# Kernel optimization log

Hardware: AMD Instinct MI355X
Metric: run time of the kernel (lower is better)

## Reference

```python
import jax, jax.numpy as jnp
import numpy as np

B, N, E = 16, 4096, 65536
IN, H = 256, 512
G1, G2 = 32, 32
M1, M2 = 1024, 32768
GOD = 8
BN_EPS = 1e-5


def setup_inputs() -> dict:
    key = jax.random.key(0)
    ks = jax.random.split(key, 16)
    rn = lambda i, sh, s=0.05: jax.random.normal(ks[i], sh, dtype=jnp.float32) * s
    return {
        "x": jax.random.normal(ks[0], (B, IN), dtype=jnp.float32),
        "smoothed_vert_pos": jax.random.normal(ks[1], (B, N * 3), dtype=jnp.float32),
        "hidden": jnp.zeros((B, H), jnp.float32),
        "edge_index": jax.random.randint(ks[2], (2, E), 0, N),
        "W0": rn(3, (G1, 3), 0.3), "a0_src": rn(4, (G1,), 0.3), "a0_dst": rn(5, (G1,), 0.3), "b0": jnp.zeros((G1,), jnp.float32),
        "W1": rn(6, (G2, G1), 0.2), "a1_src": rn(7, (G2,), 0.2), "a1_dst": rn(8, (G2,), 0.2), "b1": jnp.zeros((G2,), jnp.float32),
        "w_ih": rn(9, (3 * H, IN)), "w_hh": rn(10, (3 * H, H)),
        "b_ih": jnp.zeros((3 * H,), jnp.float32), "b_hh": jnp.zeros((3 * H,), jnp.float32),
        "lin1_w": rn(11, (M1, H)), "lin1_b": jnp.zeros((M1,), jnp.float32),
        "prelu1": jnp.full((M1,), 0.25, jnp.float32), "bn1_g": jnp.ones((M1,), jnp.float32), "bn1_b": jnp.zeros((M1,), jnp.float32),
        "lin2_w": rn(12, (M2, M1), 0.02), "lin2_b": jnp.zeros((M2,), jnp.float32),
        "prelu2": jnp.full((M2,), 0.25, jnp.float32), "bn2_g": jnp.ones((M2,), jnp.float32), "bn2_b": jnp.zeros((M2,), jnp.float32),
        "w_out": rn(13, (3, G2 + GOD), 0.2), "b_out": jnp.zeros((3,), jnp.float32),
    }


def _gat(v, src, dst, W, a_s, a_d, b):
    # PyG GATConv, heads=1, eval mode (no dropout), self-loops already in src/dst
    h = v @ W.T                                           # [N, F]
    e = jax.nn.leaky_relu((h * a_s).sum(-1)[src] + (h * a_d).sum(-1)[dst], 0.2)  # [E+N]
    m = jax.ops.segment_max(e, dst, num_segments=N)       # segment-softmax over incoming edges
    w = jnp.exp(e - m[dst])
    s = jax.ops.segment_sum(w, dst, num_segments=N)
    coef = w / s[dst]
    return jax.ops.segment_sum(coef[:, None] * h[src], dst, num_segments=N) + b


def _mlp_layer(t, w, bb, p, g, be):
    t = t @ w.T + bb                                      # Linear
    t = jnp.where(t >= 0, t, p * t)                       # PReLU (per-channel)
    # eval BatchNorm1d with running_mean=0, running_var=1
    return (t / jnp.sqrt(1.0 + BN_EPS)) * g + be


def reference(x, smoothed_vert_pos, hidden, edge_index,
              W0, a0_src, a0_dst, b0, W1, a1_src, a1_dst, b1,
              w_ih, w_hh, b_ih, b_hh,
              lin1_w, lin1_b, prelu1, bn1_g, bn1_b,
              lin2_w, lin2_b, prelu2, bn2_g, bn2_b,
              w_out, b_out):
    sv = smoothed_vert_pos.reshape(B, N, 3)
    loop = jnp.arange(N, dtype=edge_index.dtype)
    src = jnp.concatenate([edge_index[0], loop])          # GATConv add_self_loops=True
    dst = jnp.concatenate([edge_index[1], loop])
    gat0 = jax.vmap(lambda v: _gat(v, src, dst, W0, a0_src, a0_dst, b0))(sv)   # [B,N,G1]
    gat1 = jax.vmap(lambda v: _gat(v, src, dst, W1, a1_src, a1_dst, b1))(gat0)  # [B,N,G2]

    # GRUCell
    gi = x @ w_ih.T + b_ih
    gh = hidden @ w_hh.T + b_hh
    ir, iz, inn = jnp.split(gi, 3, axis=-1)
    hr, hz, hn = jnp.split(gh, 3, axis=-1)
    r = jax.nn.sigmoid(ir + hr)
    z = jax.nn.sigmoid(iz + hz)
    n = jnp.tanh(inn + r * hn)
    next_hidden = (1.0 - z) * n + z * hidden              # [B,H]

    o = _mlp_layer(next_hidden, lin1_w, lin1_b, prelu1, bn1_g, bn1_b)
    o = _mlp_layer(o, lin2_w, lin2_b, prelu2, bn2_g, bn2_b)
    gru_out = o.reshape(B, N, GOD)

    y = (jnp.concatenate([gru_out, gat1], axis=2) @ w_out.T + b_out).reshape(B, -1)
    return y, next_hidden
```

## Files before the change

### kernel.cpp

```cpp
#include <hip/hip_runtime.h>

#define BB 16
#define NN 4096
#define EE 65536
#define HH 512
#define M1N 1024
#define M2N 32768
#define CAP 96



__global__ void k_pre(int* __restrict__ cnt,
                      const float* __restrict__ x, const float* __restrict__ hid,
                      const float* __restrict__ w_ih, const float* __restrict__ w_hh,
                      const float* __restrict__ b_ih, const float* __restrict__ b_hh,
                      float* __restrict__ nh, float* __restrict__ out_nh,
                      const float* __restrict__ svp, const float* __restrict__ W0,
                      const float* __restrict__ a0s, const float* __restrict__ a0d,
                      float* __restrict__ h0t, float* __restrict__ as0t,
                      float* __restrict__ ad0t) {
  const int bid = blockIdx.x;
  if (bid < 16) {
    cnt[bid * 256 + threadIdx.x] = 0;
    return;
  }
  if (bid < 2064) {
    int wid = (bid - 16) * 4 + (threadIdx.x >> 6);
    int lane = threadIdx.x & 63;
    int b = wid >> 9, j = wid & 511;
    const float* xb = x + b * 256;
    const float* hb = hid + b * HH;
    float ir = 0.f, iz = 0.f, in_ = 0.f, hr = 0.f, hz = 0.f, hn = 0.f;
    for (int k = lane; k < 256; k += 64) {
      float xv = xb[k];
      ir  += xv * w_ih[(size_t)j * 256 + k];
      iz  += xv * w_ih[(size_t)(j + 512) * 256 + k];
      in_ += xv * w_ih[(size_t)(j + 1024) * 256 + k];
    }
    for (int k = lane; k < 512; k += 64) {
      float hv = hb[k];
      hr += hv * w_hh[(size_t)j * 512 + k];
      hz += hv * w_hh[(size_t)(j + 512) * 512 + k];
      hn += hv * w_hh[(size_t)(j + 1024) * 512 + k];
    }
#pragma unroll
    for (int m = 1; m < 64; m <<= 1) {
      ir += __shfl_xor(ir, m, 64); iz += __shfl_xor(iz, m, 64); in_ += __shfl_xor(in_, m, 64);
      hr += __shfl_xor(hr, m, 64); hz += __shfl_xor(hz, m, 64); hn  += __shfl_xor(hn, m, 64);
    }
    if (lane == 0) {
      ir += b_ih[j]; iz += b_ih[j + 512]; in_ += b_ih[j + 1024];
      hr += b_hh[j]; hz += b_hh[j + 512]; hn += b_hh[j + 1024];
      float r = 1.f / (1.f + __expf(-(ir + hr)));
      float z = 1.f / (1.f + __expf(-(iz + hz)));
      float n = tanhf(in_ + r * hn);
      float v = (1.f - z) * n + z * hb[j];
      nh[wid] = v;
      out_nh[wid] = v;
    }
    return;
  }
  int gid = (bid - 2064) * 256 + threadIdx.x;
  int grp = gid >> 5, f = gid & 31;
  int b = grp >> 12, n = grp & 4095;
  const float* v = svp + (size_t)grp * 3;
  float hv = v[0] * W0[f * 3] + v[1] * W0[f * 3 + 1] + v[2] * W0[f * 3 + 2];
  h0t[(size_t)n * 512 + b * 32 + f] = hv;
  float ps = hv * a0s[f], pd = hv * a0d[f];
#pragma unroll
  for (int m = 1; m < 32; m <<= 1) {
    ps += __shfl_xor(ps, m, 64);
    pd += __shfl_xor(pd, m, 64);
  }
  if (f == 0) { as0t[n * 16 + b] = ps; ad0t[n * 16 + b] = pd; }
}


__global__ void k_fill2(const int* __restrict__ src, const int* __restrict__ dst,
                        int* __restrict__ cnt, int* __restrict__ csr) {
  int k = blockIdx.x * 256 + threadIdx.x;
  if (k < EE) {
    int d = dst[k];
    int slot = atomicAdd(&cnt[d], 1);
    if ((unsigned)slot < CAP) csr[d * CAP + slot] = src[k];
  }
}


__global__ void k_mid(const int* __restrict__ cnt, const int* __restrict__ csr,
                      const float* __restrict__ h0t, const float* __restrict__ as0t,
                      const float* __restrict__ ad0t, const float* __restrict__ b0,
                      const float* __restrict__ W1, const float* __restrict__ a1s,
                      const float* __restrict__ a1d,
                      float* __restrict__ h1t, float* __restrict__ as1t,
                      float* __restrict__ ad1t,
                      const float* __restrict__ nh, const float* __restrict__ l1w,
                      const float* __restrict__ l1b, const float* __restrict__ p1,
                      const float* __restrict__ g1v, const float* __restrict__ be1,
                      float* __restrict__ o1) {
  const int bid = blockIdx.x;
  const int wave = threadIdx.x >> 6;
  const int lane = threadIdx.x & 63;
  if (bid < 2048) {
    __shared__ float lds[4][8][36];
    const int n  = bid * 2 + (wave >> 1);
    const int bh = wave & 1;
    const int bl = lane >> 3;
    const int fq = lane & 7;
    const int b  = bh * 8 + bl;
    const int f0 = fq * 4;
    const int deg = min(cnt[n], CAP);
    const int base = n * CAP;
    const float adn = ad0t[n * 16 + b];
    const int total = deg + 1;
    float4 acc = {0.f, 0.f, 0.f, 0.f};
    float asum = 0.f;
    for (int i = 0; i < total; i += 4) {
      int sv0, sv1, sv2, sv3;
      {
        int r0 = csr[base + i];
        int r1 = csr[base + i + 1];
        int r2 = csr[base + i + 2];
        int r3 = csr[base + i + 3];
        sv0 = (i     < deg) ? r0 : n;
        sv1 = (i + 1 < deg) ? r1 : n;
        sv2 = (i + 2 < deg) ? r2 : n;
        sv3 = (i + 3 < deg) ? r3 : n;
      }
      float e0 = as0t[sv0 * 16 + b];
      float e1 = as0t[sv1 * 16 + b];
      float e2 = as0t[sv2 * 16 + b];
      float e3 = as0t[sv3 * 16 + b];
      float4 hv0 = *(const float4*)(h0t + (size_t)sv0 * 512 + b * 32 + f0);
      float4 hv1 = *(const float4*)(h0t + (size_t)sv1 * 512 + b * 32 + f0);
      float4 hv2 = *(const float4*)(h0t + (size_t)sv2 * 512 + b * 32 + f0);
      float4 hv3 = *(const float4*)(h0t + (size_t)sv3 * 512 + b * 32 + f0);
      float e, w;
      e = e0 + adn; e = e >= 0.f ? e : 0.2f * e;
      w = (i     < total) ? __expf(e) : 0.f;
      asum += w; acc.x += w*hv0.x; acc.y += w*hv0.y; acc.z += w*hv0.z; acc.w += w*hv0.w;
      e = e1 + adn; e = e >= 0.f ? e : 0.2f * e;
      w = (i + 1 < total) ? __expf(e) : 0.f;
      asum += w; acc.x += w*hv1.x; acc.y += w*hv1.y; acc.z += w*hv1.z; acc.w += w*hv1.w;
      e = e2 + adn; e = e >= 0.f ? e : 0.2f * e;
      w = (i + 2 < total) ? __expf(e) : 0.f;
      asum += w; acc.x += w*hv2.x; acc.y += w*hv2.y; acc.z += w*hv2.z; acc.w += w*hv2.w;
      e = e3 + adn; e = e >= 0.f ? e : 0.2f * e;
      w = (i + 3 < total) ? __expf(e) : 0.f;
      asum += w; acc.x += w*hv3.x; acc.y += w*hv3.y; acc.z += w*hv3.z; acc.w += w*hv3.w;
    }
    float inv = 1.f / asum;
    float4 b0v = *(const float4*)(b0 + f0);
    float4 g0;
    g0.x = acc.x * inv + b0v.x; g0.y = acc.y * inv + b0v.y;
    g0.z = acc.z * inv + b0v.z; g0.w = acc.w * inv + b0v.w;
    *(float4*)&lds[wave][bl][f0] = g0;
    __syncthreads();
    float h1a = 0.f, h1b = 0.f, h1c = 0.f, h1d = 0.f;
    const float* gr = lds[wave][bl];
    const float* w1r = W1 + f0 * 32;
#pragma unroll
    for (int k = 0; k < 32; ++k) {
      float gk = gr[k];
      h1a += gk * w1r[k];
      h1b += gk * w1r[32 + k];
      h1c += gk * w1r[64 + k];
      h1d += gk * w1r[96 + k];
    }
    float4 h1v = {h1a, h1b, h1c, h1d};
    *(float4*)(h1t + (size_t)n * 512 + b * 32 + f0) = h1v;
    float ps = h1a * a1s[f0] + h1b * a1s[f0+1] + h1c * a1s[f0+2] + h1d * a1s[f0+3];
    float pd = h1a * a1d[f0] + h1b * a1d[f0+1] + h1c * a1d[f0+2] + h1d * a1d[f0+3];
#pragma unroll
    for (int m = 1; m < 8; m <<= 1) {
      ps += __shfl_xor(ps, m, 64);
      pd += __shfl_xor(pd, m, 64);
    }
    if (fq == 0) { as1t[n * 16 + b] = ps; ad1t[n * 16 + b] = pd; }
    return;
  }
  int wid = (bid - 2048) * 4 + wave;
  int b = wid >> 10, j = wid & 1023;
  const float* hb = nh + b * HH;
  const float* wr = l1w + (size_t)j * HH;
  float acc = 0.f;
  for (int k = lane; k < HH; k += 64) acc += hb[k] * wr[k];
#pragma unroll
  for (int m = 1; m < 64; m <<= 1) acc += __shfl_xor(acc, m, 64);
  if (lane == 0) {
    float t = acc + l1b[j];
    t = t >= 0.f ? t : p1[j] * t;
    o1[wid] = t * 0.99999500003749973f * g1v[j] + be1[j];
  }
}


__global__ __launch_bounds__(256, 4) void k_lin2(
    const float* __restrict__ o1, const float* __restrict__ w,
    const float* __restrict__ bias, const float* __restrict__ pr,
    const float* __restrict__ g, const float* __restrict__ be,
    float* __restrict__ o2) {
  const int wave = threadIdx.x >> 6;
  const int lane = threadIdx.x & 63;
  const int bh = lane >> 5;
  const int kl = lane & 31;
  const int j0 = (blockIdx.x * 4 + wave) * 4;
  const float* ob = o1 + (size_t)bh * 8 * 1024;
  const float* w0 = w + (size_t)j0 * 1024;
  float acc[4][8];
#pragma unroll
  for (int r = 0; r < 4; r++)
#pragma unroll
    for (int b = 0; b < 8; b++) acc[r][b] = 0.f;
#pragma unroll 1
  for (int it = 0; it < 8; ++it) {
    const int kq = it * 128 + kl * 4;
    float4 wv0 = *(const float4*)(w0 + kq);
    float4 wv1 = *(const float4*)(w0 + 1024 + kq);
    float4 wv2 = *(const float4*)(w0 + 2048 + kq);
    float4 wv3 = *(const float4*)(w0 + 3072 + kq);
#pragma unroll
    for (int b = 0; b < 8; b++) {
      float4 v = *(const float4*)(ob + b * 1024 + kq);
      acc[0][b] += wv0.x*v.x + wv0.y*v.y + wv0.z*v.z + wv0.w*v.w;
      acc[1][b] += wv1.x*v.x + wv1.y*v.y + wv1.z*v.z + wv1.w*v.w;
      acc[2][b] += wv2.x*v.x + wv2.y*v.y + wv2.z*v.z + wv2.w*v.w;
      acc[3][b] += wv3.x*v.x + wv3.y*v.y + wv3.z*v.z + wv3.w*v.w;
    }
  }
#pragma unroll
  for (int r = 0; r < 4; r++)
#pragma unroll
    for (int b = 0; b < 8; b++)
#pragma unroll
      for (int m = 1; m < 32; m <<= 1)
        acc[r][b] += __shfl_xor(acc[r][b], m, 64);
  if (kl == 0) {
    const float INV = 0.99999500003749973f;
#pragma unroll
    for (int r = 0; r < 4; r++) {
      const int j = j0 + r;
      const float bj = bias[j], pj = pr[j], gj = g[j], bej = be[j];
#pragma unroll
      for (int b = 0; b < 8; b++) {
        float t = acc[r][b] + bj;
        t = t >= 0.f ? t : pj * t;
        o2[(size_t)(bh * 8 + b) * M2N + j] = t * INV * gj + bej;
      }
    }
  }
}


__global__ void k_fin(const int* __restrict__ cnt, const int* __restrict__ csr,
                      const float* __restrict__ h1t, const float* __restrict__ as1t,
                      const float* __restrict__ ad1t, const float* __restrict__ b1,
                      const float* __restrict__ o2, const float* __restrict__ wout,
                      const float* __restrict__ bout, float* __restrict__ y) {
  const int wave = threadIdx.x >> 6;
  const int lane = threadIdx.x & 63;
  const int n  = blockIdx.x * 2 + (wave >> 1);
  const int bh = wave & 1;
  const int bl = lane >> 3;
  const int fq = lane & 7;
  const int b  = bh * 8 + bl;
  const int f0 = fq * 4;
  const int deg = min(cnt[n], CAP);
  const int base = n * CAP;
  const float adn = ad1t[n * 16 + b];
  const int total = deg + 1;
  float4 acc = {0.f, 0.f, 0.f, 0.f};
  float asum = 0.f;
  for (int i = 0; i < total; i += 4) {
    int sv0, sv1, sv2, sv3;
    {
      int r0 = csr[base + i];
      int r1 = csr[base + i + 1];
      int r2 = csr[base + i + 2];
      int r3 = csr[base + i + 3];
      sv0 = (i     < deg) ? r0 : n;
      sv1 = (i + 1 < deg) ? r1 : n;
      sv2 = (i + 2 < deg) ? r2 : n;
      sv3 = (i + 3 < deg) ? r3 : n;
    }
    float e0 = as1t[sv0 * 16 + b];
    float e1 = as1t[sv1 * 16 + b];
    float e2 = as1t[sv2 * 16 + b];
    float e3 = as1t[sv3 * 16 + b];
    float4 hv0 = *(const float4*)(h1t + (size_t)sv0 * 512 + b * 32 + f0);
    float4 hv1 = *(const float4*)(h1t + (size_t)sv1 * 512 + b * 32 + f0);
    float4 hv2 = *(const float4*)(h1t + (size_t)sv2 * 512 + b * 32 + f0);
    float4 hv3 = *(const float4*)(h1t + (size_t)sv3 * 512 + b * 32 + f0);
    float e, w;
    e = e0 + adn; e = e >= 0.f ? e : 0.2f * e;
    w = (i     < total) ? __expf(e) : 0.f;
    asum += w; acc.x += w*hv0.x; acc.y += w*hv0.y; acc.z += w*hv0.z; acc.w += w*hv0.w;
    e = e1 + adn; e = e >= 0.f ? e : 0.2f * e;
    w = (i + 1 < total) ? __expf(e) : 0.f;
    asum += w; acc.x += w*hv1.x; acc.y += w*hv1.y; acc.z += w*hv1.z; acc.w += w*hv1.w;
    e = e2 + adn; e = e >= 0.f ? e : 0.2f * e;
    w = (i + 2 < total) ? __expf(e) : 0.f;
    asum += w; acc.x += w*hv2.x; acc.y += w*hv2.y; acc.z += w*hv2.z; acc.w += w*hv2.w;
    e = e3 + adn; e = e >= 0.f ? e : 0.2f * e;
    w = (i + 3 < total) ? __expf(e) : 0.f;
    asum += w; acc.x += w*hv3.x; acc.y += w*hv3.y; acc.z += w*hv3.z; acc.w += w*hv3.w;
  }
  float inv = 1.f / asum;
  float4 b1v = *(const float4*)(b1 + f0);
  float gx = acc.x * inv + b1v.x, gy = acc.y * inv + b1v.y;
  float gz = acc.z * inv + b1v.z, gw = acc.w * inv + b1v.w;
  float pc0 = gx*wout[ 8+f0] + gy*wout[ 9+f0] + gz*wout[10+f0] + gw*wout[11+f0];
  float pc1 = gx*wout[48+f0] + gy*wout[49+f0] + gz*wout[50+f0] + gw*wout[51+f0];
  float pc2 = gx*wout[88+f0] + gy*wout[89+f0] + gz*wout[90+f0] + gw*wout[91+f0];
#pragma unroll
  for (int m = 1; m < 8; m <<= 1) {
    pc0 += __shfl_xor(pc0, m, 64);
    pc1 += __shfl_xor(pc1, m, 64);
    pc2 += __shfl_xor(pc2, m, 64);
  }
  if (fq == 0) {
    const float* gr = o2 + (size_t)b * M2N + n * 8;
    float4 ga = *(const float4*)gr;
    float4 gb = *(const float4*)(gr + 4);
    float c0 = pc0 + bout[0], c1 = pc1 + bout[1], c2 = pc2 + bout[2];
    c0 += ga.x*wout[0]  + ga.y*wout[1]  + ga.z*wout[2]  + ga.w*wout[3]
        + gb.x*wout[4]  + gb.y*wout[5]  + gb.z*wout[6]  + gb.w*wout[7];
    c1 += ga.x*wout[40] + ga.y*wout[41] + ga.z*wout[42] + ga.w*wout[43]
        + gb.x*wout[44] + gb.y*wout[45] + gb.z*wout[46] + gb.w*wout[47];
    c2 += ga.x*wout[80] + ga.y*wout[81] + ga.z*wout[82] + ga.w*wout[83]
        + gb.x*wout[84] + gb.y*wout[85] + gb.z*wout[86] + gb.w*wout[87];
    float* yp = y + (size_t)b * (NN * 3) + n * 3;
    yp[0] = c0; yp[1] = c1; yp[2] = c2;
  }
}


extern "C" void kernel_launch(void* const* d_in, const int* in_sizes, int n_in,
                              void* d_out, int out_size, void* d_ws, size_t ws_size,
                              hipStream_t stream) {
  const float* x    = (const float*)d_in[0];
  const float* svp  = (const float*)d_in[1];
  const float* hid  = (const float*)d_in[2];
  const int*   ei   = (const int*)d_in[3];
  const float* W0   = (const float*)d_in[4];
  const float* a0s  = (const float*)d_in[5];
  const float* a0d  = (const float*)d_in[6];
  const float* b0   = (const float*)d_in[7];
  const float* W1   = (const float*)d_in[8];
  const float* a1s  = (const float*)d_in[9];
  const float* a1d  = (const float*)d_in[10];
  const float* b1   = (const float*)d_in[11];
  const float* w_ih = (const float*)d_in[12];
  const float* w_hh = (const float*)d_in[13];
  const float* b_ih = (const float*)d_in[14];
  const float* b_hh = (const float*)d_in[15];
  const float* l1w  = (const float*)d_in[16];
  const float* l1b  = (const float*)d_in[17];
  const float* p1   = (const float*)d_in[18];
  const float* g1v  = (const float*)d_in[19];
  const float* be1  = (const float*)d_in[20];
  const float* l2w  = (const float*)d_in[21];
  const float* l2b  = (const float*)d_in[22];
  const float* p2   = (const float*)d_in[23];
  const float* g2v  = (const float*)d_in[24];
  const float* be2  = (const float*)d_in[25];
  const float* wout = (const float*)d_in[26];
  const float* bout = (const float*)d_in[27];
  float* out = (float*)d_out;

  char* ws = (char*)d_ws;
  size_t off = 0;
  auto alloc = [&](size_t bytes) -> char* {
    char* p = ws + off;
    off += (bytes + 255) & ~(size_t)255;
    return p;
  };
  int*   cnt   = (int*)alloc((size_t)NN * 4);
  int*   csr   = (int*)alloc(((size_t)NN * CAP + 16) * 4);
  float* h0t   = (float*)alloc((size_t)NN * 16 * 32 * 4);
  float* as0t  = (float*)alloc((size_t)NN * 16 * 4);
  float* ad0t  = (float*)alloc((size_t)NN * 16 * 4);
  float* h1t   = (float*)alloc((size_t)NN * 16 * 32 * 4);
  float* as1t  = (float*)alloc((size_t)NN * 16 * 4);
  float* ad1t  = (float*)alloc((size_t)NN * 16 * 4);
  float* nh    = (float*)alloc((size_t)BB * HH * 4);
  float* o1    = (float*)alloc((size_t)BB * M1N * 4);
  float* o2    = (float*)alloc((size_t)BB * M2N * 4);

  const int* srcv = ei;
  const int* dstv = ei + EE;

  k_pre<<<16 + 2048 + 8192, 256, 0, stream>>>(
      cnt, x, hid, w_ih, w_hh, b_ih, b_hh, nh, out + (size_t)BB * NN * 3,
      svp, W0, a0s, a0d, h0t, as0t, ad0t);
  k_fill2<<<EE / 256, 256, 0, stream>>>(srcv, dstv, cnt, csr);
  k_mid<<<2048 + 4096, 256, 0, stream>>>(
      cnt, csr, h0t, as0t, ad0t, b0, W1, a1s, a1d, h1t, as1t, ad1t,
      nh, l1w, l1b, p1, g1v, be1, o1);
  k_lin2<<<M2N / 16, 256, 0, stream>>>(o1, l2w, l2b, p2, g2v, be2, o2);
  k_fin<<<2048, 256, 0, stream>>>(cnt, csr, h1t, as1t, ad1t, b1, o2, wout, bout, out);
}
```

Baseline: 127.2 us.

## Regroup independent stages into fewer kernels to cut launch count

Reorganizes the kernel schedule. The lin1 GEMV now shares a kernel with CSR fill. The lin2 GEMV shares a kernel with GAT layer 0 aggregation. This takes the pipeline from five launches to four and lets independent branches overlap within each launch. The cost is that k_mid2 now applies launch_bounds(256,4) and shared memory to the GAT blocks too, which may constrain registers or occupancy for that branch.

```diff
diff --git a/kernel.cpp b/kernel.cpp
--- a/kernel.cpp
+++ b/kernel.cpp
@@ -76,9 +76,32 @@
 }
 
 
-__global__ void k_fill2(const int* __restrict__ src, const int* __restrict__ dst,
-                        int* __restrict__ cnt, int* __restrict__ csr) {
-  int k = blockIdx.x * 256 + threadIdx.x;
+__global__ void k_mid1(const float* __restrict__ nh, const float* __restrict__ l1w,
+                       const float* __restrict__ l1b, const float* __restrict__ p1,
+                       const float* __restrict__ g1v, const float* __restrict__ be1,
+                       float* __restrict__ o1,
+                       const int* __restrict__ src, const int* __restrict__ dst,
+                       int* __restrict__ cnt, int* __restrict__ csr) {
+  const int bid = blockIdx.x;
+  if (bid < 4096) {
+    const int wave = threadIdx.x >> 6;
+    const int lane = threadIdx.x & 63;
+    int wid = bid * 4 + wave;
+    int b = wid >> 10, j = wid & 1023;
+    const float* hb = nh + b * HH;
+    const float* wr = l1w + (size_t)j * HH;
+    float acc = 0.f;
+    for (int k = lane; k < HH; k += 64) acc += hb[k] * wr[k];
+#pragma unroll
+    for (int m = 1; m < 64; m <<= 1) acc += __shfl_xor(acc, m, 64);
+    if (lane == 0) {
+      float t = acc + l1b[j];
+      t = t >= 0.f ? t : p1[j] * t;
+      o1[wid] = t * 0.99999500003749973f * g1v[j] + be1[j];
+    }
+    return;
+  }
+  int k = (bid - 4096) * 256 + threadIdx.x;
   if (k < EE) {
     int d = dst[k];
     int slot = atomicAdd(&cnt[d], 1);
@@ -87,168 +110,145 @@
 }
 
 
-__global__ void k_mid(const int* __restrict__ cnt, const int* __restrict__ csr,
-                      const float* __restrict__ h0t, const float* __restrict__ as0t,
-                      const float* __restrict__ ad0t, const float* __restrict__ b0,
-                      const float* __restrict__ W1, const float* __restrict__ a1s,
-                      const float* __restrict__ a1d,
-                      float* __restrict__ h1t, float* __restrict__ as1t,
-                      float* __restrict__ ad1t,
-                      const float* __restrict__ nh, const float* __restrict__ l1w,
-                      const float* __restrict__ l1b, const float* __restrict__ p1,
-                      const float* __restrict__ g1v, const float* __restrict__ be1,
-                      float* __restrict__ o1) {
+__global__ __launch_bounds__(256, 4) void k_mid2(
+    const float* __restrict__ o1, const float* __restrict__ l2w,
+    const float* __restrict__ l2b, const float* __restrict__ p2,
+    const float* __restrict__ g2v, const float* __restrict__ be2,
+    float* __restrict__ o2,
+    const int* __restrict__ cnt, const int* __restrict__ csr,
+    const float* __restrict__ h0t, const float* __restrict__ as0t,
+    const float* __restrict__ ad0t, const float* __restrict__ b0,
+    const float* __restrict__ W1, const float* __restrict__ a1s,
+    const float* __restrict__ a1d,
+    float* __restrict__ h1t, float* __restrict__ as1t,
+    float* __restrict__ ad1t) {
   const int bid = blockIdx.x;
   const int wave = threadIdx.x >> 6;
   const int lane = threadIdx.x & 63;
+  __shared__ float lds[4][8][36];
   if (bid < 2048) {
-    __shared__ float lds[4][8][36];
-    const int n  = bid * 2 + (wave >> 1);
-    const int bh = wave & 1;
-    const int bl = lane >> 3;
-    const int fq = lane & 7;
-    const int b  = bh * 8 + bl;
-    const int f0 = fq * 4;
-    const int deg = min(cnt[n], CAP);
-    const int base = n * CAP;
-    const float adn = ad0t[n * 16 + b];
-    const int total = deg + 1;
-    float4 acc = {0.f, 0.f, 0.f, 0.f};
-    float asum = 0.f;
-    for (int i = 0; i < total; i += 4) {
-      int sv0, sv1, sv2, sv3;
-      {
-        int r0 = csr[base + i];
-        int r1 = csr[base + i + 1];
-        int r2 = csr[base + i + 2];
-        int r3 = csr[base + i + 3];
-        sv0 = (i     < deg) ? r0 : n;
-        sv1 = (i + 1 < deg) ? r1 : n;
-        sv2 = (i + 2 < deg) ? r2 : n;
-        sv3 = (i + 3 < deg) ? r3 : n;
+    const int bh = lane >> 5;
+    const int kl = lane & 31;
+    const int j0 = (bid * 4 + wave) * 4;
+    const float* ob = o1 + (size_t)bh * 8 * 1024;
+    const float* w0 = l2w + (size_t)j0 * 1024;
+    float acc[4][8];
+#pragma unroll
+    for (int r = 0; r < 4; r++)
+#pragma unroll
+      for (int b = 0; b < 8; b++) acc[r][b] = 0.f;
+#pragma unroll 1
+    for (int it = 0; it < 8; ++it) {
+      const int kq = it * 128 + kl * 4;
+      float4 wv0 = *(const float4*)(w0 + kq);
+      float4 wv1 = *(const float4*)(w0 + 1024 + kq);
+      float4 wv2 = *(const float4*)(w0 + 2048 + kq);
+      float4 wv3 = *(const float4*)(w0 + 3072 + kq);
+#pragma unroll
+      for (int b = 0; b < 8; b++) {
+        float4 v = *(const float4*)(ob + b * 1024 + kq);
+        acc[0][b] += wv0.x*v.x + wv0.y*v.y + wv0.z*v.z + wv0.w*v.w;
+        acc[1][b] += wv1.x*v.x + wv1.y*v.y + wv1.z*v.z + wv1.w*v.w;
+        acc[2][b] += wv2.x*v.x + wv2.y*v.y + wv2.z*v.z + wv2.w*v.w;
+        acc[3][b] += wv3.x*v.x + wv3.y*v.y + wv3.z*v.z + wv3.w*v.w;
       }
-      float e0 = as0t[sv0 * 16 + b];
-      float e1 = as0t[sv1 * 16 + b];
-      float e2 = as0t[sv2 * 16 + b];
-      float e3 = as0t[sv3 * 16 + b];
-      float4 hv0 = *(const float4*)(h0t + (size_t)sv0 * 512 + b * 32 + f0);
-      float4 hv1 = *(const float4*)(h0t + (size_t)sv1 * 512 + b * 32 + f0);
-      float4 hv2 = *(const float4*)(h0t + (size_t)sv2 * 512 + b * 32 + f0);
-      float4 hv3 = *(const float4*)(h0t + (size_t)sv3 * 512 + b * 32 + f0);
-      float e, w;
-      e = e0 + adn; e = e >= 0.f ? e : 0.2f * e;
-      w = (i     < total) ? __expf(e) : 0.f;
-      asum += w; acc.x += w*hv0.x; acc.y += w*hv0.y; acc.z += w*hv0.z; acc.w += w*hv0.w;
-      e = e1 + adn; e = e >= 0.f ? e : 0.2f * e;
-      w = (i + 1 < total) ? __expf(e) : 0.f;
-      asum += w; acc.x += w*hv1.x; acc.y += w*hv1.y; acc.z += w*hv1.z; acc.w += w*hv1.w;
-      e = e2 + adn; e = e >= 0.f ? e : 0.2f * e;
-      w = (i + 2 < total) ? __expf(e) : 0.f;
-      asum += w; acc.x += w*hv2.x; acc.y += w*hv2.y; acc.z += w*hv2.z; acc.w += w*hv2.w;
-      e = e3 + adn; e = e >= 0.f ? e : 0.2f * e;
-      w = (i + 3 < total) ? __expf(e) : 0.f;
-      asum += w; acc.x += w*hv3.x; acc.y += w*hv3.y; acc.z += w*hv3.z; acc.w += w*hv3.w;
-    }
-    float inv = 1.f / asum;
-    float4 b0v = *(const float4*)(b0 + f0);
-    float4 g0;
-    g0.x = acc.x * inv + b0v.x; g0.y = acc.y * inv + b0v.y;
-    g0.z = acc.z * inv + b0v.z; g0.w = acc.w * inv + b0v.w;
-    *(float4*)&lds[wave][bl][f0] = g0;
-    __syncthreads();
-    float h1a = 0.f, h1b = 0.f, h1c = 0.f, h1d = 0.f;
-    const float* gr = lds[wave][bl];
-    const float* w1r = W1 + f0 * 32;
-#pragma unroll
-    for (int k = 0; k < 32; ++k) {
-      float gk = gr[k];
-      h1a += gk * w1r[k];
-      h1b += gk * w1r[32 + k];
-      h1c += gk * w1r[64 + k];
-      h1d += gk * w1r[96 + k];
-    }
-    float4 h1v = {h1a, h1b, h1c, h1d};
-    *(float4*)(h1t + (size_t)n * 512 + b * 32 + f0) = h1v;
-    float ps = h1a * a1s[f0] + h1b * a1s[f0+1] + h1c * a1s[f0+2] + h1d * a1s[f0+3];
-    float pd = h1a * a1d[f0] + h1b * a1d[f0+1] + h1c * a1d[f0+2] + h1d * a1d[f0+3];
-#pragma unroll
-    for (int m = 1; m < 8; m <<= 1) {
-      ps += __shfl_xor(ps, m, 64);
-      pd += __shfl_xor(pd, m, 64);
-    }
-    if (fq == 0) { as1t[n * 16 + b] = ps; ad1t[n * 16 + b] = pd; }
+    }
+#pragma unroll
+    for (int r = 0; r < 4; r++)
+#pragma unroll
+      for (int b = 0; b < 8; b++)
+#pragma unroll
+        for (int m = 1; m < 32; m <<= 1)
+          acc[r][b] += __shfl_xor(acc[r][b], m, 64);
+    if (kl == 0) {
+      const float INV = 0.99999500003749973f;
+#pragma unroll
+      for (int r = 0; r < 4; r++) {
+        const int j = j0 + r;
+        const float bj = l2b[j], pj = p2[j], gj = g2v[j], bej = be2[j];
+#pragma unroll
+        for (int b = 0; b < 8; b++) {
+          float t = acc[r][b] + bj;
+          t = t >= 0.f ? t : pj * t;
+          o2[(size_t)(bh * 8 + b) * M2N + j] = t * INV * gj + bej;
+        }
+      }
+    }
     return;
   }
-  int wid = (bid - 2048) * 4 + wave;
-  int b = wid >> 10, j = wid & 1023;
-  const float* hb = nh + b * HH;
-  const float* wr = l1w + (size_t)j * HH;
-  float acc = 0.f;
-  for (int k = lane; k < HH; k += 64) acc += hb[k] * wr[k];
-#pragma unroll
-  for (int m = 1; m < 64; m <<= 1) acc += __shfl_xor(acc, m, 64);
-  if (lane == 0) {
-    float t = acc + l1b[j];
-    t = t >= 0.f ? t : p1[j] * t;
-    o1[wid] = t * 0.99999500003749973f * g1v[j] + be1[j];
-  }
-}
-
-
-__global__ __launch_bounds__(256, 4) void k_lin2(
-    const float* __restrict__ o1, const float* __restrict__ w,
-    const float* __restrict__ bias, const float* __restrict__ pr,
-    const float* __restrict__ g, const float* __restrict__ be,
-    float* __restrict__ o2) {
-  const int wave = threadIdx.x >> 6;
-  const int lane = threadIdx.x & 63;
-  const int bh = lane >> 5;
-  const int kl = lane & 31;
-  const int j0 = (blockIdx.x * 4 + wave) * 4;
-  const float* ob = o1 + (size_t)bh * 8 * 1024;
-  const float* w0 = w + (size_t)j0 * 1024;
-  float acc[4][8];
-#pragma unroll
-  for (int r = 0; r < 4; r++)
-#pragma unroll
-    for (int b = 0; b < 8; b++) acc[r][b] = 0.f;
-#pragma unroll 1
-  for (int it = 0; it < 8; ++it) {
-    const int kq = it * 128 + kl * 4;
-    float4 wv0 = *(const float4*)(w0 + kq);
-    float4 wv1 = *(const float4*)(w0 + 1024 + kq);
-    float4 wv2 = *(const float4*)(w0 + 2048 + kq);
-    float4 wv3 = *(const float4*)(w0 + 3072 + kq);
-#pragma unroll
-    for (int b = 0; b < 8; b++) {
-      float4 v = *(const float4*)(ob + b * 1024 + kq);
-      acc[0][b] += wv0.x*v.x + wv0.y*v.y + wv0.z*v.z + wv0.w*v.w;
-      acc[1][b] += wv1.x*v.x + wv1.y*v.y + wv1.z*v.z + wv1.w*v.w;
-      acc[2][b] += wv2.x*v.x + wv2.y*v.y + wv2.z*v.z + wv2.w*v.w;
-      acc[3][b] += wv3.x*v.x + wv3.y*v.y + wv3.z*v.z + wv3.w*v.w;
-    }
-  }
-#pragma unroll
-  for (int r = 0; r < 4; r++)
-#pragma unroll
-    for (int b = 0; b < 8; b++)
-#pragma unroll
-      for (int m = 1; m < 32; m <<= 1)
-        acc[r][b] += __shfl_xor(acc[r][b], m, 64);
-  if (kl == 0) {
-    const float INV = 0.99999500003749973f;
-#pragma unroll
-    for (int r = 0; r < 4; r++) {
-      const int j = j0 + r;
-      const float bj = bias[j], pj = pr[j], gj = g[j], bej = be[j];
-#pragma unroll
-      for (int b = 0; b < 8; b++) {
-        float t = acc[r][b] + bj;
-        t = t >= 0.f ? t : pj * t;
-        o2[(size_t)(bh * 8 + b) * M2N + j] = t * INV * gj + bej;
-      }
-    }
-  }
+  const int u  = bid - 2048;
+  const int n  = u * 2 + (wave >> 1);
+  const int bh = wave & 1;
+  const int bl = lane >> 3;
+  const int fq = lane & 7;
+  const int b  = bh * 8 + bl;
+  const int f0 = fq * 4;
+  const int boff = b * 32 + f0;
+  const int deg = min(cnt[n], CAP);
+  const int base = n * CAP;
+  const float adn = ad0t[n * 16 + b];
+  const int total = deg + 1;
+  float4 acc = {0.f, 0.f, 0.f, 0.f};
+  float asum = 0.f;
+  for (int i = 0; i < total; i += 4) {
+    int r0 = csr[base + i];
+    int r1 = csr[base + i + 1];
+    int r2 = csr[base + i + 2];
+    int r3 = csr[base + i + 3];
+    int sv0 = (i     < deg) ? r0 : n;
+    int sv1 = (i + 1 < deg) ? r1 : n;
+    int sv2 = (i + 2 < deg) ? r2 : n;
+    int sv3 = (i + 3 < deg) ? r3 : n;
+    float e0 = as0t[sv0 * 16 + b];
+    float e1 = as0t[sv1 * 16 + b];
+    float e2 = as0t[sv2 * 16 + b];
+    float e3 = as0t[sv3 * 16 + b];
+    float4 hv0 = *(const float4*)(h0t + (size_t)sv0 * 512 + boff);
+    float4 hv1 = *(const float4*)(h0t + (size_t)sv1 * 512 + boff);
+    float4 hv2 = *(const float4*)(h0t + (size_t)sv2 * 512 + boff);
+    float4 hv3 = *(const float4*)(h0t + (size_t)sv3 * 512 + boff);
+    float e, w;
+    e = e0 + adn; e = e >= 0.f ? e : 0.2f * e;
+    w = (i     < total) ? __expf(e) : 0.f;
+    asum += w; acc.x += w*hv0.x; acc.y += w*hv0.y; acc.z += w*hv0.z; acc.w += w*hv0.w;
+    e = e1 + adn; e = e >= 0.f ? e : 0.2f * e;
+    w = (i + 1 < total) ? __expf(e) : 0.f;
+    asum += w; acc.x += w*hv1.x; acc.y += w*hv1.y; acc.z += w*hv1.z; acc.w += w*hv1.w;
+    e = e2 + adn; e = e >= 0.f ? e : 0.2f * e;
+    w = (i + 2 < total) ? __expf(e) : 0.f;
+    asum += w; acc.x += w*hv2.x; acc.y += w*hv2.y; acc.z += w*hv2.z; acc.w += w*hv2.w;
+    e = e3 + adn; e = e >= 0.f ? e : 0.2f * e;
+    w = (i + 3 < total) ? __expf(e) : 0.f;
+    asum += w; acc.x += w*hv3.x; acc.y += w*hv3.y; acc.z += w*hv3.z; acc.w += w*hv3.w;
+  }
+  float inv = 1.f / asum;
+  float4 b0v = *(const float4*)(b0 + f0);
+  float4 g0;
+  g0.x = acc.x * inv + b0v.x; g0.y = acc.y * inv + b0v.y;
+  g0.z = acc.z * inv + b0v.z; g0.w = acc.w * inv + b0v.w;
+  *(float4*)&lds[wave][bl][f0] = g0;
+  __syncthreads();
+  float h1a = 0.f, h1b = 0.f, h1c = 0.f, h1d = 0.f;
+  const float* gr = lds[wave][bl];
+  const float* w1r = W1 + f0 * 32;
+#pragma unroll
+  for (int k = 0; k < 32; ++k) {
+    float gk = gr[k];
+    h1a += gk * w1r[k];
+    h1b += gk * w1r[32 + k];
+    h1c += gk * w1r[64 + k];
+    h1d += gk * w1r[96 + k];
+  }
+  float4 h1v = {h1a, h1b, h1c, h1d};
+  *(float4*)(h1t + (size_t)n * 512 + boff) = h1v;
+  float ps = h1a * a1s[f0] + h1b * a1s[f0+1] + h1c * a1s[f0+2] + h1d * a1s[f0+3];
+  float pd = h1a * a1d[f0] + h1b * a1d[f0+1] + h1c * a1d[f0+2] + h1d * a1d[f0+3];
+#pragma unroll
+  for (int m = 1; m < 8; m <<= 1) {
+    ps += __shfl_xor(ps, m, 64);
+    pd += __shfl_xor(pd, m, 64);
+  }
+  if (fq == 0) { as1t[n * 16 + b] = ps; ad1t[n * 16 + b] = pd; }
 }
 
 
@@ -265,6 +265,7 @@
   const int fq = lane & 7;
   const int b  = bh * 8 + bl;
   const int f0 = fq * 4;
+  const int boff = b * 32 + f0;
   const int deg = min(cnt[n], CAP);
   const int base = n * CAP;
   const float adn = ad1t[n * 16 + b];
@@ -272,25 +273,22 @@
   float4 acc = {0.f, 0.f, 0.f, 0.f};
   float asum = 0.f;
   for (int i = 0; i < total; i += 4) {
-    int sv0, sv1, sv2, sv3;
-    {
-      int r0 = csr[base + i];
-      int r1 = csr[base + i + 1];
-      int r2 = csr[base + i + 2];
-      int r3 = csr[base + i + 3];
-      sv0 = (i     < deg) ? r0 : n;
-      sv1 = (i + 1 < deg) ? r1 : n;
-      sv2 = (i + 2 < deg) ? r2 : n;
-      sv3 = (i + 3 < deg) ? r3 : n;
-    }
+    int r0 = csr[base + i];
+    int r1 = csr[base + i + 1];
+    int r2 = csr[base + i + 2];
+    int r3 = csr[base + i + 3];
+    int sv0 = (i     < deg) ? r0 : n;
+    int sv1 = (i + 1 < deg) ? r1 : n;
+    int sv2 = (i + 2 < deg) ? r2 : n;
+    int sv3 = (i + 3 < deg) ? r3 : n;
     float e0 = as1t[sv0 * 16 + b];
     float e1 = as1t[sv1 * 16 + b];
     float e2 = as1t[sv2 * 16 + b];
     float e3 = as1t[sv3 * 16 + b];
-    float4 hv0 = *(const float4*)(h1t + (size_t)sv0 * 512 + b * 32 + f0);
-    float4 hv1 = *(const float4*)(h1t + (size_t)sv1 * 512 + b * 32 + f0);
-    float4 hv2 = *(const float4*)(h1t + (size_t)sv2 * 512 + b * 32 + f0);
-    float4 hv3 = *(const float4*)(h1t + (size_t)sv3 * 512 + b * 32 + f0);
+    float4 hv0 = *(const float4*)(h1t + (size_t)sv0 * 512 + boff);
+    float4 hv1 = *(const float4*)(h1t + (size_t)sv1 * 512 + boff);
+    float4 hv2 = *(const float4*)(h1t + (size_t)sv2 * 512 + boff);
+    float4 hv3 = *(const float4*)(h1t + (size_t)sv3 * 512 + boff);
     float e, w;
     e = e0 + adn; e = e >= 0.f ? e : 0.2f * e;
     w = (i     < total) ? __expf(e) : 0.f;
@@ -393,10 +391,10 @@
   k_pre<<<16 + 2048 + 8192, 256, 0, stream>>>(
       cnt, x, hid, w_ih, w_hh, b_ih, b_hh, nh, out + (size_t)BB * NN * 3,
       svp, W0, a0s, a0d, h0t, as0t, ad0t);
-  k_fill2<<<EE / 256, 256, 0, stream>>>(srcv, dstv, cnt, csr);
-  k_mid<<<2048 + 4096, 256, 0, stream>>>(
-      cnt, csr, h0t, as0t, ad0t, b0, W1, a1s, a1d, h1t, as1t, ad1t,
-      nh, l1w, l1b, p1, g1v, be1, o1);
-  k_lin2<<<M2N / 16, 256, 0, stream>>>(o1, l2w, l2b, p2, g2v, be2, o2);
+  k_mid1<<<4096 + 256, 256, 0, stream>>>(
+      nh, l1w, l1b, p1, g1v, be1, o1, srcv, dstv, cnt, csr);
+  k_mid2<<<2048 + 2048, 256, 0, stream>>>(
+      o1, l2w, l2b, p2, g2v, be2, o2,
+      cnt, csr, h0t, as0t, ad0t, b0, W1, a1s, a1d, h1t, as1t, ad1t);
   k_fin<<<2048, 256, 0, stream>>>(cnt, csr, h1t, as1t, ad1t, b1, o2, wout, bout, out);
 }
```

New measurement: 127.1 us. No clear change (-0.1%).
